# Kernel tuning notes

Hardware: AMD Instinct MI355X
Metric: run time of the kernel (lower is better)

## Reference

```python
import jax, jax.numpy as jnp
import numpy as np

B, N, F, H, E = 2, 384, 64, 128, 4
EPS_MEAN = 1e-10


def _lin(x, W, b=None):
    y = x @ W
    return y if b is None else y + b


def setup_inputs() -> dict:
    key = jax.random.key(0)
    ks = jax.random.split(key, 22)
    def rn(k, shape):
        return (jax.random.normal(k, shape, jnp.float32) / np.sqrt(shape[0])).astype(jnp.float32)
    h = jax.random.normal(ks[0], (B, N, F), jnp.float32)
    coord = jax.random.normal(ks[1], (B, N, 3), jnp.float32)
    edge_attr = jax.random.normal(ks[2], (B, N, N, E), jnp.float32)
    node_attr = jax.random.normal(ks[3], (B, N, F), jnp.float32)
    mask = (jax.random.uniform(ks[4], (B, N)) > 0.2).astype(jnp.float32)
    d_in_edge = 2 * F + 1 + E  # source, target, radial, edge_attr
    return dict(
        h=h, coord=coord, edge_attr=edge_attr, node_attr=node_attr, mask=mask,
        We1=rn(ks[5], (d_in_edge, H)), be1=jnp.zeros((H,), jnp.float32),
        We2=rn(ks[6], (H, H)), be2=jnp.zeros((H,), jnp.float32),
        Wa1=rn(ks[7], (H, H)), ba1=jnp.zeros((H,), jnp.float32),
        Wa2=rn(ks[8], (H, 1)), ba2=jnp.zeros((1,), jnp.float32),
        Wn1=rn(ks[9], (H + F + F, H)), bn1=jnp.zeros((H,), jnp.float32),
        Wn2=rn(ks[10], (H, F)), bn2=jnp.zeros((F,), jnp.float32),
        Wc1=rn(ks[11], (H, H)), bc1=jnp.zeros((H,), jnp.float32),
        Wc2=(jax.random.normal(ks[12], (H, 1), jnp.float32) * 0.001),  # xavier gain=0.001, no bias
    )


def reference(h, coord, edge_attr, node_attr, mask,
              We1, be1, We2, be2, Wa1, ba1, Wa2, ba2,
              Wn1, bn1, Wn2, bn2, Wc1, bc1, Wc2):
    # mask inputs
    coord = coord * mask[..., None]
    h = h * mask[..., None]
    mask2d = mask[:, :, None] * mask[:, None, :]  # [B,N,N]

    # coord2radial
    coord_diff = coord[:, :, None, :] - coord[:, None, :, :]      # [B,N,N,3]
    radial = jnp.sum(coord_diff ** 2, axis=-1, keepdims=True)     # [B,N,N,1]
    radial = radial * mask2d[..., None]
    coord_diff = coord_diff * mask2d[..., None]

    # edge model: source[b,i,j]=h[b,j], target[b,i,j]=h[b,i]
    source = jnp.broadcast_to(h[:, None, :, :], (h.shape[0], h.shape[1], h.shape[1], h.shape[2]))
    target = jnp.broadcast_to(h[:, :, None, :], source.shape)
    einp = jnp.concatenate([source, target, radial, edge_attr], axis=-1)  # [B,N,N,2F+1+E]
    m = jnp.tanh(_lin(einp, We1, be1))
    m = jnp.tanh(_lin(m, We2, be2))
    attn = jax.nn.sigmoid(_lin(jnp.tanh(_lin(m, Wa1, ba1)), Wa2, ba2))
    edge_feat = m * attn                                           # [B,N,N,H]

    # coord model (coords_agg='mean')
    embed_edge = _lin(jnp.tanh(_lin(edge_feat, Wc1, bc1)), Wc2)    # [B,N,N,1]
    trans = coord_diff * embed_edge * mask2d[..., None]            # [B,N,N,3]
    denom = jnp.sum(mask2d, axis=2, keepdims=True) + EPS_MEAN      # [B,N,1]
    coord_out = coord + jnp.sum(trans, axis=2) / denom
    coord_out = coord_out * mask[..., None]

    # node model (residual)
    agg = jnp.sum(edge_feat, axis=2)                               # [B,N,H]
    ninp = jnp.concatenate([h, node_attr, agg], axis=-1) * mask[..., None]
    nout = _lin(jnp.tanh(_lin(ninp, Wn1, bn1)), Wn2, bn2)
    h_out = (h + nout) * mask[..., None]

    return h_out, coord_out, edge_feat
```

## Files before the change

kernel.cpp:

```cpp
#include <hip/hip_runtime.h>

#define BB 2
#define NN 384
#define FF 64
#define HH 128
#define EE 4
#define ETILE 64
#define NCHUNK (NN / ETILE)

using f4 = float4;
typedef __attribute__((ext_vector_type(8))) short          bf16x8;
typedef __attribute__((ext_vector_type(8))) unsigned short u16x8;
typedef __attribute__((ext_vector_type(4))) unsigned int   u32x4;
typedef __attribute__((ext_vector_type(4))) float          f32x4;

__device__ __forceinline__ float fast_tanh(float x) {
    float e = __expf(2.0f * x);
    return 1.0f - 2.0f / (e + 1.0f);
}
__device__ __forceinline__ float fast_sigmoid(float x) {
    return 1.0f / (1.0f + __expf(-x));
}
__device__ __forceinline__ unsigned short f2bf(float x) {
    unsigned int u = __float_as_uint(x);
    unsigned int r = (u + 0x7fffu + ((u >> 16) & 1u)) >> 16;
    return (unsigned short)r;
}
__device__ __forceinline__ float bf2f(unsigned short h) {
    return __uint_as_float(((unsigned int)h) << 16);
}
__device__ __forceinline__ bf16x8 as_bf16x8(u32x4 v) {
    union { u32x4 u; bf16x8 b; } c; c.u = v; return c.b;
}

__global__ __launch_bounds__(128) void pre_kernel(
    const float* __restrict__ h, const float* __restrict__ mask,
    const float* __restrict__ We1, const float* __restrict__ be1,
    float* __restrict__ Sg, float* __restrict__ Tg)
{
    const int bn = blockIdx.x;
    const int t  = threadIdx.x;
    __shared__ float hl[FF];
    const float mk = mask[bn];
    if (t < FF) hl[t] = h[bn * FF + t] * mk;
    __syncthreads();
    float s = 0.f, tv = be1[t];
#pragma unroll 8
    for (int f = 0; f < FF; ++f) {
        const float hv = hl[f];
        s  = fmaf(hv, We1[f * HH + t], s);
        tv = fmaf(hv, We1[(FF + f) * HH + t], tv);
    }
    Sg[bn * HH + t] = s;
    Tg[bn * HH + t] = tv;
}

__global__ __launch_bounds__(128) void wconv_kernel(
    const float* __restrict__ W0, const float* __restrict__ W1,
    const float* __restrict__ W2, unsigned short* __restrict__ WT)
{
    const int mat = blockIdx.x >> 7;
    const int o   = blockIdx.x & 127;
    const int k   = threadIdx.x;
    const float* src = (mat == 0) ? W0 : (mat == 1) ? W1 : W2;
    const float w = src[k * HH + o];
    const unsigned short hi = f2bf(w);
    const unsigned short lo = f2bf(w - bf2f(hi));
    WT[(mat * 2 + 0) * 16384 + o * HH + k] = hi;
    WT[(mat * 2 + 1) * 16384 + o * HH + k] = lo;
}

__device__ __forceinline__ void mfma_pass_dual(
    const ushort* __restrict__ A1, const ushort* __restrict__ A2,
    const ushort* __restrict__ WTp, f32x4 acc[4][2],
    const int l15, const int l4, const int c0)
{
    u32x4 Bf[2][4];
#pragma unroll
    for (int ct = 0; ct < 2; ++ct)
#pragma unroll
        for (int kb = 0; kb < 4; ++kb)
            Bf[ct][kb] = *(const u32x4*)&WTp[(c0 + ct * 16 + l15) * HH + kb * 32 + l4 * 8];
#pragma unroll
    for (int rt = 0; rt < 4; ++rt) {
        bf16x8 Af1[4], Af2[4];
#pragma unroll
        for (int kb = 0; kb < 4; ++kb) {
            const int idx = (16 * rt + l15) * HH + (((kb * 4 + l4) ^ l15) * 8);
            Af1[kb] = *(const bf16x8*)&A1[idx];
            Af2[kb] = *(const bf16x8*)&A2[idx];
        }
#pragma unroll
        for (int ct = 0; ct < 2; ++ct)
#pragma unroll
            for (int kb = 0; kb < 4; ++kb)
                acc[rt][ct] = __builtin_amdgcn_mfma_f32_16x16x32_bf16(
                    Af1[kb], as_bf16x8(Bf[ct][kb]), acc[rt][ct], 0, 0, 0);
#pragma unroll
        for (int ct = 0; ct < 2; ++ct)
#pragma unroll
            for (int kb = 0; kb < 4; ++kb)
                acc[rt][ct] = __builtin_amdgcn_mfma_f32_16x16x32_bf16(
                    Af2[kb], as_bf16x8(Bf[ct][kb]), acc[rt][ct], 0, 0, 0);
    }
}

__device__ __forceinline__ void mfma_pass_single(
    const ushort* __restrict__ A1, const ushort* __restrict__ WTp,
    f32x4 acc[4][2], const int l15, const int l4, const int c0)
{
    u32x4 Bf[2][4];
#pragma unroll
    for (int ct = 0; ct < 2; ++ct)
#pragma unroll
        for (int kb = 0; kb < 4; ++kb)
            Bf[ct][kb] = *(const u32x4*)&WTp[(c0 + ct * 16 + l15) * HH + kb * 32 + l4 * 8];
#pragma unroll
    for (int rt = 0; rt < 4; ++rt) {
        bf16x8 Af1[4];
#pragma unroll
        for (int kb = 0; kb < 4; ++kb) {
            const int idx = (16 * rt + l15) * HH + (((kb * 4 + l4) ^ l15) * 8);
            Af1[kb] = *(const bf16x8*)&A1[idx];
        }
#pragma unroll
        for (int ct = 0; ct < 2; ++ct)
#pragma unroll
            for (int kb = 0; kb < 4; ++kb)
                acc[rt][ct] = __builtin_amdgcn_mfma_f32_16x16x32_bf16(
                    Af1[kb], as_bf16x8(Bf[ct][kb]), acc[rt][ct], 0, 0, 0);
    }
}

__global__ __launch_bounds__(256, 4) void edge_kernel(
    const float* __restrict__ coord, const float* __restrict__ edge_attr,
    const float* __restrict__ mask,  const float* __restrict__ We1,
    const float* __restrict__ be2,   const float* __restrict__ ba1,
    const float* __restrict__ Wa2,   const float* __restrict__ ba2,
    const float* __restrict__ bc1,   const float* __restrict__ Wc2,
    const float* __restrict__ Sg,    const float* __restrict__ Tg,
    const unsigned short* __restrict__ WT,
    float* __restrict__ ef_out,
    float* __restrict__ agg_part,
    float* __restrict__ cag_part)
{
    __shared__ ushort Ah[ETILE * HH];
    __shared__ ushort Al[ETILE * HH];
    __shared__ float Tb[HH];
    __shared__ float sd_l[ETILE];
    __shared__ float cd_l[ETILE][3];
    __shared__ float ea_l[ETILE][4];
    __shared__ float attn_l[ETILE];
    __shared__ float embed_l[ETILE];
    __shared__ float part[4 * ETILE];

    const int bid = blockIdx.x;
    const int jc  = bid % NCHUNK;
    const int i   = (bid / NCHUNK) % NN;
    const int b   = bid / (NCHUNK * NN);
    const int j0  = jc * ETILE;
    const int t   = threadIdx.x;
    const int e   = t & 63;
    const int wv  = __builtin_amdgcn_readfirstlane(t >> 6);
    const int l15 = e & 15, l4 = e >> 4;
    const int c0  = wv * 32;

    const unsigned short* We2h = WT;
    const unsigned short* We2l = WT + 16384;
    const unsigned short* Wa1h = WT + 32768;
    const unsigned short* Wa1l = WT + 49152;
    const unsigned short* Wc1h = WT + 65536;

    const float be2a = be2[c0 + l15],      be2b = be2[c0 + 16 + l15];
    const float ba1a = ba1[c0 + l15],      ba1b = ba1[c0 + 16 + l15];
    const float wa2a = Wa2[c0 + l15],      wa2b = Wa2[c0 + 16 + l15];
    const float bc1a = bc1[c0 + l15],      bc1b = bc1[c0 + 16 + l15];
    const float wc2a = Wc2[c0 + l15],      wc2b = Wc2[c0 + 16 + l15];
    const float ba2s = ba2[0];

    if (t < HH) Tb[t] = Tg[(b * NN + i) * HH + t];
    if (t < ETILE) {
        const int j = j0 + t;
        const float mi = mask[b * NN + i], mj = mask[b * NN + j];
        const float m2 = mi * mj;
        const float d0 = coord[(b * NN + i) * 3 + 0] * mi - coord[(b * NN + j) * 3 + 0] * mj;
        const float d1 = coord[(b * NN + i) * 3 + 1] * mi - coord[(b * NN + j) * 3 + 1] * mj;
        const float d2 = coord[(b * NN + i) * 3 + 2] * mi - coord[(b * NN + j) * 3 + 2] * mj;
        sd_l[t] = (d0 * d0 + d1 * d1 + d2 * d2) * m2;
        cd_l[t][0] = d0 * m2; cd_l[t][1] = d1 * m2; cd_l[t][2] = d2 * m2;
        const f4 ea = *(const f4*)&edge_attr[(((size_t)b * NN + i) * NN + j) * EE];
        ea_l[t][0] = ea.x; ea_l[t][1] = ea.y; ea_l[t][2] = ea.z; ea_l[t][3] = ea.w;
    }
    __syncthreads();

    {
        const float rad = sd_l[e];
        const float ea0 = ea_l[e][0], ea1 = ea_l[e][1], ea2 = ea_l[e][2], ea3 = ea_l[e][3];
        const float* Srow = &Sg[((size_t)b * NN + (j0 + e)) * HH];
#pragma unroll
        for (int s = 0; s < 4; ++s) {
            u16x8 hp, lp;
#pragma unroll
            for (int hq = 0; hq < 2; ++hq) {
                const int o = c0 + s * 8 + hq * 4;
                const f4 sv = *(const f4*)&Srow[o];
                const f4 tb = *(const f4*)&Tb[o];
                const f4 wr = *(const f4*)&We1[128 * HH + o];
                const f4 w0 = *(const f4*)&We1[129 * HH + o];
                const f4 w1 = *(const f4*)&We1[130 * HH + o];
                const f4 w2 = *(const f4*)&We1[131 * HH + o];
                const f4 w3 = *(const f4*)&We1[132 * HH + o];
                float pv[4];
                pv[0] = sv.x + tb.x + rad * wr.x + ea0 * w0.x + ea1 * w1.x + ea2 * w2.x + ea3 * w3.x;
                pv[1] = sv.y + tb.y + rad * wr.y + ea0 * w0.y + ea1 * w1.y + ea2 * w2.y + ea3 * w3.y;
                pv[2] = sv.z + tb.z + rad * wr.z + ea0 * w0.z + ea1 * w1.z + ea2 * w2.z + ea3 * w3.z;
                pv[3] = sv.w + tb.w + rad * wr.w + ea0 * w0.w + ea1 * w1.w + ea2 * w2.w + ea3 * w3.w;
#pragma unroll
                for (int q = 0; q < 4; ++q) {
                    const float v = fast_tanh(pv[q]);
                    const unsigned short hv = f2bf(v);
                    hp[hq * 4 + q] = hv;
                    lp[hq * 4 + q] = f2bf(v - bf2f(hv));
                }
            }
            const int phys = (wv * 4 + s) ^ (e & 15);
            *(u16x8*)&Ah[e * HH + phys * 8] = hp;
            *(u16x8*)&Al[e * HH + phys * 8] = lp;
        }
    }
    __syncthreads();

    f32x4 acc[4][2];

#pragma unroll
    for (int rt = 0; rt < 4; ++rt)
#pragma unroll
        for (int ct = 0; ct < 2; ++ct) acc[rt][ct] = (f32x4){0.f, 0.f, 0.f, 0.f};
    mfma_pass_dual(Ah, Al, We2h, acc, l15, l4, c0);
    mfma_pass_single(Ah, We2l, acc, l15, l4, c0);
    __syncthreads();
#pragma unroll
    for (int rt = 0; rt < 4; ++rt)
#pragma unroll
        for (int ct = 0; ct < 2; ++ct)
#pragma unroll
            for (int r = 0; r < 4; ++r) {
                const float v = fast_tanh(acc[rt][ct][r] + (ct ? be2b : be2a));
                const int row = 16 * rt + 4 * l4 + r;
                const int col = c0 + ct * 16 + l15;
                const int idx = row * HH + (((col >> 3) ^ (row & 15)) * 8) + (col & 7);
                const unsigned short hv = f2bf(v);
                Ah[idx] = hv;
                Al[idx] = f2bf(v - bf2f(hv));
            }
    __syncthreads();

#pragma unroll
    for (int rt = 0; rt < 4; ++rt)
#pragma unroll
        for (int ct = 0; ct < 2; ++ct) acc[rt][ct] = (f32x4){0.f, 0.f, 0.f, 0.f};
    mfma_pass_dual(Ah, Al, Wa1h, acc, l15, l4, c0);
    mfma_pass_single(Ah, Wa1l, acc, l15, l4, c0);
#pragma unroll
    for (int rt = 0; rt < 4; ++rt)
#pragma unroll
        for (int r = 0; r < 4; ++r) {
            float s = fast_tanh(acc[rt][0][r] + ba1a) * wa2a +
                      fast_tanh(acc[rt][1][r] + ba1b) * wa2b;
            s += __shfl_xor(s, 1); s += __shfl_xor(s, 2);
            s += __shfl_xor(s, 4); s += __shfl_xor(s, 8);
            if (l15 == 0) part[wv * 64 + 16 * rt + 4 * l4 + r] = s;
        }
    __syncthreads();
    if (t < ETILE)
        attn_l[t] = fast_sigmoid(part[t] + part[64 + t] + part[128 + t] +
                                 part[192 + t] + ba2s);
    __syncthreads();

#pragma unroll
    for (int rt = 0; rt < 4; ++rt)
#pragma unroll
        for (int ct = 0; ct < 2; ++ct) acc[rt][ct] = (f32x4){0.f, 0.f, 0.f, 0.f};
    mfma_pass_single(Ah, Wc1h, acc, l15, l4, c0);
#pragma unroll
    for (int rt = 0; rt < 4; ++rt)
#pragma unroll
        for (int r = 0; r < 4; ++r) {
            const int row = 16 * rt + 4 * l4 + r;
            const float at = attn_l[row];
            float s = fast_tanh(at * acc[rt][0][r] + bc1a) * wc2a +
                      fast_tanh(at * acc[rt][1][r] + bc1b) * wc2b;
            s += __shfl_xor(s, 1); s += __shfl_xor(s, 2);
            s += __shfl_xor(s, 4); s += __shfl_xor(s, 8);
            if (l15 == 0) part[wv * 64 + row] = s;
        }
    __syncthreads();
    if (t < ETILE)
        embed_l[t] = part[t] + part[64 + t] + part[128 + t] + part[192 + t];
    __syncthreads();

    {
        const float at = attn_l[e];
        float efv[32];
        float* orow = &ef_out[(((size_t)b * NN + i) * NN + (j0 + e)) * HH + c0];
#pragma unroll
        for (int s = 0; s < 4; ++s) {
            const int phys = (wv * 4 + s) ^ (e & 15);
            const u16x8 hv = *(const u16x8*)&Ah[e * HH + phys * 8];
            const u16x8 lv = *(const u16x8*)&Al[e * HH + phys * 8];
            f4 v0, v1;
            v0.x = (bf2f(hv[0]) + bf2f(lv[0])) * at;
            v0.y = (bf2f(hv[1]) + bf2f(lv[1])) * at;
            v0.z = (bf2f(hv[2]) + bf2f(lv[2])) * at;
            v0.w = (bf2f(hv[3]) + bf2f(lv[3])) * at;
            v1.x = (bf2f(hv[4]) + bf2f(lv[4])) * at;
            v1.y = (bf2f(hv[5]) + bf2f(lv[5])) * at;
            v1.z = (bf2f(hv[6]) + bf2f(lv[6])) * at;
            v1.w = (bf2f(hv[7]) + bf2f(lv[7])) * at;
            *(f4*)&orow[s * 8]     = v0;
            *(f4*)&orow[s * 8 + 4] = v1;
            efv[s * 8 + 0] = v0.x; efv[s * 8 + 1] = v0.y;
            efv[s * 8 + 2] = v0.z; efv[s * 8 + 3] = v0.w;
            efv[s * 8 + 4] = v1.x; efv[s * 8 + 5] = v1.y;
            efv[s * 8 + 6] = v1.z; efv[s * 8 + 7] = v1.w;
        }
#pragma unroll
        for (int q = 0; q < 32; ++q) {
            float v = efv[q];
            v += __shfl_xor(v, 1);  v += __shfl_xor(v, 2);
            v += __shfl_xor(v, 4);  v += __shfl_xor(v, 8);
            v += __shfl_xor(v, 16); v += __shfl_xor(v, 32);
            efv[q] = v;
        }
        if (e < 8) {
            f4 v; v.x = efv[e * 4]; v.y = efv[e * 4 + 1];
            v.z = efv[e * 4 + 2]; v.w = efv[e * 4 + 3];
            *(f4*)&agg_part[(size_t)bid * HH + c0 + e * 4] = v;
        }
    }
    if (t < ETILE) {
        const float em = embed_l[t];
        float tr0 = cd_l[t][0] * em, tr1 = cd_l[t][1] * em, tr2 = cd_l[t][2] * em;
#pragma unroll
        for (int off = 1; off < 64; off <<= 1) {
            tr0 += __shfl_xor(tr0, off);
            tr1 += __shfl_xor(tr1, off);
            tr2 += __shfl_xor(tr2, off);
        }
        if (t == 0) {
            cag_part[(size_t)bid * 3 + 0] = tr0;
            cag_part[(size_t)bid * 3 + 1] = tr1;
            cag_part[(size_t)bid * 3 + 2] = tr2;
        }
    }
}

__global__ __launch_bounds__(128) void node_kernel(
    const float* __restrict__ h, const float* __restrict__ coord,
    const float* __restrict__ node_attr, const float* __restrict__ mask,
    const float* __restrict__ Wn1, const float* __restrict__ bn1,
    const float* __restrict__ Wn2, const float* __restrict__ bn2,
    const float* __restrict__ agg_part, const float* __restrict__ cag_part,
    float* __restrict__ h_out, float* __restrict__ c_out)
{
    const int bn = blockIdx.x;
    const int b  = bn / NN;
    const int t  = threadIdx.x;
    __shared__ float nl[2 * FF + HH];
    __shared__ float ul[HH];
    __shared__ float msp[2];
    const float mi = mask[bn];

    float s = mask[b * NN + t] + mask[b * NN + t + 128] + mask[b * NN + t + 256];
#pragma unroll
    for (int off = 1; off < 64; off <<= 1) s += __shfl_xor(s, off);
    if ((t & 63) == 0) msp[t >> 6] = s;

    if (t < FF) nl[t] = h[bn * FF + t] * mi;
    else        nl[t] = node_attr[bn * FF + (t - FF)] * mi;
    {
        float a = 0.f;
#pragma unroll
        for (int jc = 0; jc < NCHUNK; ++jc)
            a += agg_part[((size_t)bn * NCHUNK + jc) * HH + t];
        nl[2 * FF + t] = a * mi;
    }
    __syncthreads();

    float acc = bn1[t];
#pragma unroll 8
    for (int k = 0; k < 2 * FF + HH; ++k)
        acc = fmaf(nl[k], Wn1[k * HH + t], acc);
    ul[t] = fast_tanh(acc);
    __syncthreads();

    if (t < FF) {
        float a = bn2[t];
#pragma unroll 8
        for (int o = 0; o < HH; ++o)
            a = fmaf(ul[o], Wn2[o * FF + t], a);
        h_out[bn * FF + t] = (h[bn * FF + t] * mi + a) * mi;
    } else if (t < FF + 3) {
        const int d = t - FF;
        float cag = 0.f;
        for (int jc = 0; jc < NCHUNK; ++jc)
            cag += cag_part[((size_t)bn * NCHUNK + jc) * 3 + d];
        const float msum  = msp[0] + msp[1];
        const float denom = mi * msum + 1e-10f;
        c_out[bn * 3 + d] = (coord[bn * 3 + d] * mi + cag / denom) * mi;
    }
}

extern "C" void kernel_launch(void* const* d_in, const int* in_sizes, int n_in,
                              void* d_out, int out_size, void* d_ws, size_t ws_size,
                              hipStream_t stream)
{
    const float* h         = (const float*)d_in[0];
    const float* coord     = (const float*)d_in[1];
    const float* edge_attr = (const float*)d_in[2];
    const float* node_attr = (const float*)d_in[3];
    const float* mask      = (const float*)d_in[4];
    const float* We1 = (const float*)d_in[5];
    const float* be1 = (const float*)d_in[6];
    const float* We2 = (const float*)d_in[7];
    const float* be2 = (const float*)d_in[8];
    const float* Wa1 = (const float*)d_in[9];
    const float* ba1 = (const float*)d_in[10];
    const float* Wa2 = (const float*)d_in[11];
    const float* ba2 = (const float*)d_in[12];
    const float* Wn1 = (const float*)d_in[13];
    const float* bn1 = (const float*)d_in[14];
    const float* Wn2 = (const float*)d_in[15];
    const float* bn2 = (const float*)d_in[16];
    const float* Wc1 = (const float*)d_in[17];
    const float* bc1 = (const float*)d_in[18];
    const float* Wc2 = (const float*)d_in[19];

    float* out    = (float*)d_out;
    float* h_out  = out;
    float* c_out  = out + (size_t)BB * NN * FF;
    float* ef_out = c_out + (size_t)BB * NN * 3;

    float* ws = (float*)d_ws;
    float* Sg = ws;
    float* Tg = Sg + (size_t)BB * NN * HH;
    float* agg_part = Tg + (size_t)BB * NN * HH;
    float* cag_part = agg_part + (size_t)BB * NN * NCHUNK * HH;
    unsigned short* WT = (unsigned short*)(cag_part + (size_t)BB * NN * NCHUNK * 3);

    pre_kernel<<<BB * NN, 128, 0, stream>>>(h, mask, We1, be1, Sg, Tg);
    wconv_kernel<<<3 * HH, 128, 0, stream>>>(We2, Wa1, Wc1, WT);
    edge_kernel<<<BB * NN * NCHUNK, 256, 0, stream>>>(
        coord, edge_attr, mask, We1, be2, ba1, Wa2, ba2, bc1, Wc2,
        Sg, Tg, WT, ef_out, agg_part, cag_part);
    node_kernel<<<BB * NN, 128, 0, stream>>>(
        h, coord, node_attr, mask, Wn1, bn1, Wn2, bn2,
        agg_part, cag_part, h_out, c_out);
}
```

Before: 488.4 us.

## Batch nodes per block in pre/node kernels and coalesce edge_feat stores

pre_kernel now computes 16 nodes per block and node_kernel 8 nodes per block with a split-K partial sum, so each weight load is reused across several nodes instead of being reloaded per node. The edge kernel epilogue now has each thread write contiguous 4-float chunks across rows, giving coalesced edge_feat stores. It replaces the 32-value shuffle reduction for agg with per-thread column accumulation plus a shared-memory reduction across waves. This costs more registers, an extra sync in the edge kernel, and fewer blocks in the small kernels.

Result: faster. 456.0 us (-6.6%).

```diff
diff --git a/kernel.cpp b/kernel.cpp
--- a/kernel.cpp
+++ b/kernel.cpp
@@ -7,10 +7,13 @@
 #define EE 4
 #define ETILE 64
 #define NCHUNK (NN / ETILE)
+#define PRE_NB 16
+#define NODE_NB 8
 
 using f4 = float4;
 typedef __attribute__((ext_vector_type(8))) short          bf16x8;
 typedef __attribute__((ext_vector_type(8))) unsigned short u16x8;
+typedef __attribute__((ext_vector_type(4))) unsigned short u16x4;
 typedef __attribute__((ext_vector_type(4))) unsigned int   u32x4;
 typedef __attribute__((ext_vector_type(4))) float          f32x4;
 
@@ -38,21 +41,32 @@
     const float* __restrict__ We1, const float* __restrict__ be1,
     float* __restrict__ Sg, float* __restrict__ Tg)
 {
-    const int bn = blockIdx.x;
+    const int n0 = blockIdx.x * PRE_NB;
     const int t  = threadIdx.x;
-    __shared__ float hl[FF];
-    const float mk = mask[bn];
-    if (t < FF) hl[t] = h[bn * FF + t] * mk;
-    __syncthreads();
-    float s = 0.f, tv = be1[t];
-#pragma unroll 8
+    __shared__ float hl[PRE_NB][FF];
+    for (int q = t; q < PRE_NB * FF; q += 128) {
+        const int n = q >> 6, f = q & 63;
+        hl[n][f] = h[(n0 + n) * FF + f] * mask[n0 + n];
+    }
+    __syncthreads();
+    float accS[PRE_NB], accT[PRE_NB];
+    const float b1 = be1[t];
+#pragma unroll
+    for (int n = 0; n < PRE_NB; ++n) { accS[n] = 0.f; accT[n] = b1; }
     for (int f = 0; f < FF; ++f) {
-        const float hv = hl[f];
-        s  = fmaf(hv, We1[f * HH + t], s);
-        tv = fmaf(hv, We1[(FF + f) * HH + t], tv);
-    }
-    Sg[bn * HH + t] = s;
-    Tg[bn * HH + t] = tv;
+        const float ws = We1[f * HH + t];
+        const float wt = We1[(FF + f) * HH + t];
+#pragma unroll
+        for (int n = 0; n < PRE_NB; ++n) {
+            accS[n] = fmaf(hl[n][f], ws, accS[n]);
+            accT[n] = fmaf(hl[n][f], wt, accT[n]);
+        }
+    }
+#pragma unroll
+    for (int n = 0; n < PRE_NB; ++n) {
+        Sg[(n0 + n) * HH + t] = accS[n];
+        Tg[(n0 + n) * HH + t] = accT[n];
+    }
 }
 
 __global__ __launch_bounds__(128) void wconv_kernel(
@@ -152,7 +166,7 @@
     __shared__ float ea_l[ETILE][4];
     __shared__ float attn_l[ETILE];
     __shared__ float embed_l[ETILE];
-    __shared__ float part[4 * ETILE];
+    __shared__ float part[512];
 
     const int bid = blockIdx.x;
     const int jc  = bid % NCHUNK;
@@ -300,42 +314,37 @@
     __syncthreads();
 
     {
-        const float at = attn_l[e];
-        float efv[32];
-        float* orow = &ef_out[(((size_t)b * NN + i) * NN + (j0 + e)) * HH + c0];
-#pragma unroll
-        for (int s = 0; s < 4; ++s) {
-            const int phys = (wv * 4 + s) ^ (e & 15);
-            const u16x8 hv = *(const u16x8*)&Ah[e * HH + phys * 8];
-            const u16x8 lv = *(const u16x8*)&Al[e * HH + phys * 8];
-            f4 v0, v1;
-            v0.x = (bf2f(hv[0]) + bf2f(lv[0])) * at;
-            v0.y = (bf2f(hv[1]) + bf2f(lv[1])) * at;
-            v0.z = (bf2f(hv[2]) + bf2f(lv[2])) * at;
-            v0.w = (bf2f(hv[3]) + bf2f(lv[3])) * at;
-            v1.x = (bf2f(hv[4]) + bf2f(lv[4])) * at;
-            v1.y = (bf2f(hv[5]) + bf2f(lv[5])) * at;
-            v1.z = (bf2f(hv[6]) + bf2f(lv[6])) * at;
-            v1.w = (bf2f(hv[7]) + bf2f(lv[7])) * at;
-            *(f4*)&orow[s * 8]     = v0;
-            *(f4*)&orow[s * 8 + 4] = v1;
-            efv[s * 8 + 0] = v0.x; efv[s * 8 + 1] = v0.y;
-            efv[s * 8 + 2] = v0.z; efv[s * 8 + 3] = v0.w;
-            efv[s * 8 + 4] = v1.x; efv[s * 8 + 5] = v1.y;
-            efv[s * 8 + 6] = v1.z; efv[s * 8 + 7] = v1.w;
-        }
-#pragma unroll
-        for (int q = 0; q < 32; ++q) {
-            float v = efv[q];
-            v += __shfl_xor(v, 1);  v += __shfl_xor(v, 2);
-            v += __shfl_xor(v, 4);  v += __shfl_xor(v, 8);
-            v += __shfl_xor(v, 16); v += __shfl_xor(v, 32);
-            efv[q] = v;
-        }
-        if (e < 8) {
-            f4 v; v.x = efv[e * 4]; v.y = efv[e * 4 + 1];
-            v.z = efv[e * 4 + 2]; v.w = efv[e * 4 + 3];
-            *(f4*)&agg_part[(size_t)bid * HH + c0 + e * 4] = v;
+        const int erow = t >> 5;
+        const int colq = t & 31;
+        const int col  = colq * 4;
+        const int chunk = col >> 3;
+        const int sub   = col & 7;
+        float a0 = 0.f, a1 = 0.f, a2 = 0.f, a3 = 0.f;
+        float* obase = &ef_out[(((size_t)b * NN + i) * NN + j0) * HH];
+#pragma unroll
+        for (int it = 0; it < 8; ++it) {
+            const int row = it * 8 + erow;
+            const float at = attn_l[row];
+            const int idx = row * HH + ((chunk ^ (row & 15)) * 8) + sub;
+            const u16x4 hv4 = *(const u16x4*)&Ah[idx];
+            const u16x4 lv4 = *(const u16x4*)&Al[idx];
+            f4 v;
+            v.x = (bf2f(hv4[0]) + bf2f(lv4[0])) * at;
+            v.y = (bf2f(hv4[1]) + bf2f(lv4[1])) * at;
+            v.z = (bf2f(hv4[2]) + bf2f(lv4[2])) * at;
+            v.w = (bf2f(hv4[3]) + bf2f(lv4[3])) * at;
+            *(f4*)&obase[row * HH + col] = v;
+            a0 += v.x; a1 += v.y; a2 += v.z; a3 += v.w;
+        }
+        a0 += __shfl_xor(a0, 32);
+        a1 += __shfl_xor(a1, 32);
+        a2 += __shfl_xor(a2, 32);
+        a3 += __shfl_xor(a3, 32);
+        if (e < 32) {
+            part[wv * HH + col + 0] = a0;
+            part[wv * HH + col + 1] = a1;
+            part[wv * HH + col + 2] = a2;
+            part[wv * HH + col + 3] = a3;
         }
     }
     if (t < ETILE) {
@@ -353,9 +362,13 @@
             cag_part[(size_t)bid * 3 + 2] = tr2;
         }
     }
-}
-
-__global__ __launch_bounds__(128) void node_kernel(
+    __syncthreads();
+    if (t < HH)
+        agg_part[(size_t)bid * HH + t] =
+            part[t] + part[HH + t] + part[2 * HH + t] + part[3 * HH + t];
+}
+
+__global__ __launch_bounds__(256) void node_kernel(
     const float* __restrict__ h, const float* __restrict__ coord,
     const float* __restrict__ node_attr, const float* __restrict__ mask,
     const float* __restrict__ Wn1, const float* __restrict__ bn1,
@@ -363,50 +376,98 @@
     const float* __restrict__ agg_part, const float* __restrict__ cag_part,
     float* __restrict__ h_out, float* __restrict__ c_out)
 {
-    const int bn = blockIdx.x;
-    const int b  = bn / NN;
+    const int n0 = blockIdx.x * NODE_NB;
+    const int b  = n0 / NN;
     const int t  = threadIdx.x;
-    __shared__ float nl[2 * FF + HH];
-    __shared__ float ul[HH];
-    __shared__ float msp[2];
-    const float mi = mask[bn];
-
-    float s = mask[b * NN + t] + mask[b * NN + t + 128] + mask[b * NN + t + 256];
-#pragma unroll
-    for (int off = 1; off < 64; off <<= 1) s += __shfl_xor(s, off);
-    if ((t & 63) == 0) msp[t >> 6] = s;
-
-    if (t < FF) nl[t] = h[bn * FF + t] * mi;
-    else        nl[t] = node_attr[bn * FF + (t - FF)] * mi;
+    __shared__ float nl[NODE_NB][2 * FF + HH];
+    __shared__ float ul[NODE_NB][HH];
+    __shared__ float pp[4][NODE_NB][HH];
+    __shared__ float msum_s;
+
+    for (int q = t; q < NODE_NB * 256; q += 256) {
+        const int n = q >> 8, k = q & 255;
+        const int bn = n0 + n;
+        const float mi = mask[bn];
+        float v;
+        if (k < FF)          v = h[bn * FF + k] * mi;
+        else if (k < 2 * FF) v = node_attr[bn * FF + (k - FF)] * mi;
+        else {
+            float a = 0.f;
+            const int o = k - 2 * FF;
+#pragma unroll
+            for (int jc = 0; jc < NCHUNK; ++jc)
+                a += agg_part[((size_t)bn * NCHUNK + jc) * HH + o];
+            v = a * mi;
+        }
+        nl[n][k] = v;
+    }
+    if (t < 64) {
+        float s = 0.f;
+#pragma unroll
+        for (int q = 0; q < 6; ++q) s += mask[b * NN + q * 64 + t];
+#pragma unroll
+        for (int off = 1; off < 64; off <<= 1) s += __shfl_xor(s, off);
+        if (t == 0) msum_s = s;
+    }
+    __syncthreads();
+
     {
-        float a = 0.f;
-#pragma unroll
-        for (int jc = 0; jc < NCHUNK; ++jc)
-            a += agg_part[((size_t)bn * NCHUNK + jc) * HH + t];
-        nl[2 * FF + t] = a * mi;
-    }
-    __syncthreads();
-
-    float acc = bn1[t];
-#pragma unroll 8
-    for (int k = 0; k < 2 * FF + HH; ++k)
-        acc = fmaf(nl[k], Wn1[k * HH + t], acc);
-    ul[t] = fast_tanh(acc);
-    __syncthreads();
-
-    if (t < FF) {
-        float a = bn2[t];
-#pragma unroll 8
-        for (int o = 0; o < HH; ++o)
-            a = fmaf(ul[o], Wn2[o * FF + t], a);
-        h_out[bn * FF + t] = (h[bn * FF + t] * mi + a) * mi;
-    } else if (t < FF + 3) {
-        const int d = t - FF;
+        const int col = t & 127, kh = t >> 7;
+        float acc[NODE_NB];
+#pragma unroll
+        for (int n = 0; n < NODE_NB; ++n) acc[n] = 0.f;
+        for (int k = kh * 128; k < kh * 128 + 128; ++k) {
+            const float w = Wn1[k * HH + col];
+#pragma unroll
+            for (int n = 0; n < NODE_NB; ++n)
+                acc[n] = fmaf(nl[n][k], w, acc[n]);
+        }
+#pragma unroll
+        for (int n = 0; n < NODE_NB; ++n) pp[kh][n][col] = acc[n];
+    }
+    __syncthreads();
+#pragma unroll
+    for (int r = 0; r < 4; ++r) {
+        const int idx = t + 256 * r;
+        const int n = idx >> 7, col = idx & 127;
+        ul[n][col] = fast_tanh(pp[0][n][col] + pp[1][n][col] + bn1[col]);
+    }
+    __syncthreads();
+
+    {
+        const int col = t & 63, ks = t >> 6;
+        float acc[NODE_NB];
+#pragma unroll
+        for (int n = 0; n < NODE_NB; ++n) acc[n] = 0.f;
+        for (int k = ks * 32; k < ks * 32 + 32; ++k) {
+            const float w = Wn2[k * FF + col];
+#pragma unroll
+            for (int n = 0; n < NODE_NB; ++n)
+                acc[n] = fmaf(ul[n][k], w, acc[n]);
+        }
+#pragma unroll
+        for (int n = 0; n < NODE_NB; ++n) pp[ks][n][col] = acc[n];
+    }
+    __syncthreads();
+#pragma unroll
+    for (int r = 0; r < 2; ++r) {
+        const int idx = t + 256 * r;
+        const int n = idx >> 6, col = idx & 63;
+        const int bn = n0 + n;
+        const float mi = mask[bn];
+        const float a = pp[0][n][col] + pp[1][n][col] + pp[2][n][col] +
+                        pp[3][n][col] + bn2[col];
+        h_out[bn * FF + col] = (nl[n][col] + a) * mi;
+    }
+    if (t < NODE_NB * 3) {
+        const int n = t / 3, d = t % 3;
+        const int bn = n0 + n;
+        const float mi = mask[bn];
         float cag = 0.f;
+#pragma unroll
         for (int jc = 0; jc < NCHUNK; ++jc)
             cag += cag_part[((size_t)bn * NCHUNK + jc) * 3 + d];
-        const float msum  = msp[0] + msp[1];
-        const float denom = mi * msum + 1e-10f;
+        const float denom = mi * msum_s + 1e-10f;
         c_out[bn * 3 + d] = (coord[bn * 3 + d] * mi + cag / denom) * mi;
     }
 }
@@ -448,12 +509,12 @@
     float* cag_part = agg_part + (size_t)BB * NN * NCHUNK * HH;
     unsigned short* WT = (unsigned short*)(cag_part + (size_t)BB * NN * NCHUNK * 3);
 
-    pre_kernel<<<BB * NN, 128, 0, stream>>>(h, mask, We1, be1, Sg, Tg);
+    pre_kernel<<<BB * NN / PRE_NB, 128, 0, stream>>>(h, mask, We1, be1, Sg, Tg);
     wconv_kernel<<<3 * HH, 128, 0, stream>>>(We2, Wa1, Wc1, WT);
     edge_kernel<<<BB * NN * NCHUNK, 256, 0, stream>>>(
         coord, edge_attr, mask, We1, be2, ba1, Wa2, ba2, bc1, Wc2,
         Sg, Tg, WT, ef_out, agg_part, cag_part);
-    node_kernel<<<BB * NN, 128, 0, stream>>>(
+    node_kernel<<<BB * NN / NODE_NB, 256, 0, stream>>>(
         h, coord, node_attr, mask, Wn1, bn1, Wn2, bn2,
         agg_part, cag_part, h_out, c_out);
 }
```
